# Kernel optimization log

Measured on AMD Instinct MI355X. Metric: run time of the kernel, lower is better.

Reference implementation:

```python
import jax, jax.numpy as jnp
import numpy as np

K = 3
PAD = 1
STRIDE = 1
DIL = 1


def _conv_offset(x, w, b):
    # standard 3x3 conv, NCHW
    out = jax.lax.conv_general_dilated(
        x, w, window_strides=(STRIDE, STRIDE), padding=((PAD, PAD), (PAD, PAD)),
        rhs_dilation=(DIL, DIL), dimension_numbers=('NCHW', 'OIHW', 'NCHW'))
    return out + b[None, :, None, None]


def _bilinear_sample(x, px, py):
    # x: (b,c,h,w); px,py: (b,N) absolute pixel coords; zero padding outside.
    b, c, h, w = x.shape
    x_flat = x.reshape(b, c, h * w)
    x0 = jnp.floor(px)
    y0 = jnp.floor(py)
    wx1 = px - x0
    wy1 = py - y0
    wx0 = 1.0 - wx1
    wy0 = 1.0 - wy1

    def gather(xi, yi, wt):
        valid = (xi >= 0) & (xi <= w - 1) & (yi >= 0) & (yi <= h - 1)
        xc = jnp.clip(xi, 0, w - 1).astype(jnp.int32)
        yc = jnp.clip(yi, 0, h - 1).astype(jnp.int32)
        idx = yc * w + xc  # (b,N)
        v = jax.vmap(lambda xf, i: jnp.take(xf, i, axis=1))(x_flat, idx)  # (b,c,N)
        return v * (wt * valid.astype(x.dtype))[:, None, :]

    out = gather(x0, y0, wy0 * wx0)
    out = out + gather(x0 + 1, y0, wy0 * wx1)
    out = out + gather(x0, y0 + 1, wy1 * wx0)
    out = out + gather(x0 + 1, y0 + 1, wy1 * wx1)
    return out


def setup_inputs() -> dict:
    key = jax.random.key(0)
    k1, k2, k3, k4 = jax.random.split(key, 4)
    x = jax.random.normal(k1, (8, 64, 128, 128), dtype=jnp.float32)
    # small random offset-predictor weights (repo inits to zero; random gives nonzero offsets)
    w_off = jax.random.normal(k2, (27, 64, 3, 3), dtype=jnp.float32) * 0.01
    b_off = jax.random.normal(k3, (27,), dtype=jnp.float32) * 0.01
    w_conv = jax.random.normal(k4, (64, 576), dtype=jnp.float32) / np.sqrt(3.0 * 576.0)
    return {"x": x, "w_off": w_off, "b_off": b_off, "w_conv": w_conv}


def reference(x, w_off, b_off, w_conv):
    b, c, h, w = x.shape
    out = _conv_offset(x, w_off, b_off)  # (b, 3*K*K, H, W)
    H, W = out.shape[2], out.shape[3]
    o1, o2, m = jnp.split(out, 3, axis=1)  # each (b, K*K, H, W)
    mask = jax.nn.sigmoid(m).reshape(b, 1, K, K, H, W)
    # base grid (absolute coords), per module __init__
    x_start = DIL / 2 * (K - 1) - PAD  # = 0.0 here
    y_start = DIL / 2 * (K - 1) - PAD
    x_cood = (x_start + STRIDE * jnp.arange(W)).astype(x.dtype)
    y_cood = (y_start + STRIDE * jnp.arange(H)).astype(x.dtype)
    # per-tap kernel bias, tap order is (kh, kw) row-major
    taps = (jnp.arange(K) - (K - 1) / 2) * DIL
    x_bias = jnp.tile(taps, K).astype(x.dtype)      # (K*K,)
    y_bias = jnp.repeat(taps, K).astype(x.dtype)    # (K*K,)
    px = o1 + x_cood[None, None, None, :] + x_bias[None, :, None, None]  # (b,9,H,W)
    py = o2 + y_cood[None, None, :, None] + y_bias[None, :, None, None]
    N = K * K * H * W
    y = _bilinear_sample(x, px.reshape(b, N), py.reshape(b, N))  # (b,c,N)
    y = y.reshape(b, c, K, K, H, W) * mask
    y = y.reshape(b, c * K * K, H, W)
    # 1x1 conv == channel GEMM
    return jnp.einsum('bkhw,ok->bohw', y, w_conv)
```

## Files before the change

kernel.cpp:

```cpp
#include <hip/hip_runtime.h>
#include <math.h>

#define HW_   128
#define CIN_  64
#define IMG_  (HW_ * HW_)

#define TR_    6
#define TC_    40
#define PIT_   36
#define TILEDW (TR_ * TC_ * PIT_)
#define NU_    (TR_ * 8 * 10)

typedef short    s16x8 __attribute__((ext_vector_type(8)));
typedef float    f32x4 __attribute__((ext_vector_type(4)));
typedef float    f32x2 __attribute__((ext_vector_type(2)));
typedef unsigned u32x4 __attribute__((ext_vector_type(4)));

__device__ __forceinline__ short f2bf(float f) {
  union { float f; unsigned i; } v; v.f = f;
  unsigned r = (v.i + 0x7fffu + ((v.i >> 16) & 1u)) >> 16;
  return (short)r;
}

#if defined(__has_builtin)
#if __has_builtin(__builtin_amdgcn_cvt_pk_bf16_f32)
#define HAVE_CVT_PK_BF16 1
#endif
#endif

__device__ __forceinline__ unsigned PK2(float a, float b) {
#ifdef HAVE_CVT_PK_BF16
  typedef __bf16 bf16x2_t __attribute__((ext_vector_type(2)));
  union { bf16x2_t v; unsigned u; } cv;
  cv.v = __builtin_amdgcn_cvt_pk_bf16_f32(a, b);
  return cv.u;
#else
  union { float f; unsigned u; } ua, ub; ua.f = a; ub.f = b;
  unsigned ra = ua.u + 0x7fffu + ((ua.u >> 16) & 1u);
  unsigned rb = ub.u + 0x7fffu + ((ub.u >> 16) & 1u);
  return __builtin_amdgcn_perm(rb, ra, 0x07060302u);
#endif
}

__device__ __forceinline__ f32x2 up2d(unsigned d) {
  union { unsigned u; float f; } lo, hi;
  lo.u = d << 16; hi.u = d;
  return (f32x2){lo.f, hi.f};
}


__global__ __launch_bounds__(256) void wprep(const float* __restrict__ w_off,
                                             const float* __restrict__ w_conv,
                                             short* __restrict__ wOf,
                                             short* __restrict__ wA) {
  int t = blockIdx.x * 256 + threadIdx.x;
  if (t < 36864) {
    int i = t & 7, o = (t >> 3) & 63, q = (t >> 9) & 3, ks = (t >> 11) & 1, j = t >> 12;
    int c = ks * 32 + q * 8 + i;
    wA[t] = f2bf(w_conv[o * 576 + c * 9 + j]);
  }
  if (t < 18432) {
    int i = t & 7, m = (t >> 3) & 31, q = (t >> 8) & 3, ks = (t >> 10) & 1, j = t >> 11;
    int c = ks * 32 + q * 8 + i;
    wOf[t] = (m < 27) ? f2bf(w_off[(m * 64 + c) * 9 + j]) : (short)0;
  }
}

__global__ __launch_bounds__(256)
__attribute__((amdgpu_waves_per_eu(4)))
void dfuse(const float* __restrict__ x,
           const short* __restrict__ wOf,
           const float* __restrict__ b_off,
           const short* __restrict__ wA,
           float* __restrict__ out) {
  __shared__ __align__(16) unsigned lds_[TILEDW];

  int bi  = blockIdx.x & 7;
  int tid = blockIdx.x >> 3;
  int h0  = (tid >> 2) << 1;
  int w0  = (tid & 3) << 5;
  int t   = threadIdx.x;
  int wv  = t >> 6, l = t & 63;
  int col = l & 15, q = l >> 4;
  int px_local = wv * 16 + col;
  int rl  = px_local >> 5;
  int cl  = px_local & 31;
  int h   = h0 + rl;
  int w   = w0 + cl;
  int p   = h * HW_ + w;

  const float* xB = x + (size_t)bi * (CIN_ * IMG_);

  {
    f32x4 L0a[4], L1a[4], L0b[4], L1b[4];
    int sda, sdb;
    unsigned ma, mb;
    {
      int u = t;
      int cc = u % 10, cq = (u / 10) & 7, r = u / 80;
      int y  = h0 - 2 + r;
      int ys = min(max(y, 0), HW_ - 1);
      int xg0 = w0 - 4 + cc * 4;
      int xs  = min(max(xg0, 0), HW_ - 4);
      ma = ((y >= 0) && (y < HW_) && (xg0 >= 0) && (xg0 < HW_)) ? 0xffffffffu : 0u;
      const float* s0 = xB + (size_t)(8 * cq) * IMG_ + ys * HW_ + xs;
#pragma unroll
      for (int i = 0; i < 4; ++i) {
        L0a[i] = *(const f32x4*)(s0 + (2 * i) * IMG_);
        L1a[i] = *(const f32x4*)(s0 + (2 * i + 1) * IMG_);
      }
      sda = (r * TC_ + cc * 4) * PIT_ + cq * 4;
    }
    bool hasB = (t + 256) < NU_;
    {
      int u = hasB ? (t + 256) : 0;
      int cc = u % 10, cq = (u / 10) & 7, r = u / 80;
      int y  = h0 - 2 + r;
      int ys = min(max(y, 0), HW_ - 1);
      int xg0 = w0 - 4 + cc * 4;
      int xs  = min(max(xg0, 0), HW_ - 4);
      mb = ((y >= 0) && (y < HW_) && (xg0 >= 0) && (xg0 < HW_)) ? 0xffffffffu : 0u;
      const float* s0 = xB + (size_t)(8 * cq) * IMG_ + ys * HW_ + xs;
#pragma unroll
      for (int i = 0; i < 4; ++i) {
        L0b[i] = *(const f32x4*)(s0 + (2 * i) * IMG_);
        L1b[i] = *(const f32x4*)(s0 + (2 * i + 1) * IMG_);
      }
      sdb = (r * TC_ + cc * 4) * PIT_ + cq * 4;
    }
#pragma unroll
    for (int pxi = 0; pxi < 4; ++pxi) {
      u32x4 v;
#pragma unroll
      for (int i = 0; i < 4; ++i) v[i] = PK2(L0a[i][pxi], L1a[i][pxi]) & ma;
      *(u32x4*)(lds_ + sda + pxi * PIT_) = v;
    }
    if (hasB) {
#pragma unroll
      for (int pxi = 0; pxi < 4; ++pxi) {
        u32x4 v;
#pragma unroll
        for (int i = 0; i < 4; ++i) v[i] = PK2(L0b[i][pxi], L1b[i][pxi]) & mb;
        *(u32x4*)(lds_ + sdb + pxi * PIT_) = v;
      }
    }
  }
  __syncthreads();

  float oall[32];
  {
    const short* wq = wOf + q * 256 + col * 8;
    f32x4 a0v = {0.f, 0.f, 0.f, 0.f};
    f32x4 a1v = {0.f, 0.f, 0.f, 0.f};
    f32x4 a0w = {0.f, 0.f, 0.f, 0.f};
    f32x4 a1w = {0.f, 0.f, 0.f, 0.f};
    const unsigned* tb = &lds_[((rl + 2) * TC_ + (cl + 4)) * PIT_ + q * 4];
#pragma unroll
    for (int j = 0; j < 9; ++j) {
      int dy = j / 3 - 1, dx = j % 3 - 1;
      const unsigned* tp = tb + (dy * TC_ + dx) * PIT_;
      union { u32x4 u; s16x8 v; } B0, B1;
      B0.u = *(const u32x4*)tp;
      B1.u = *(const u32x4*)(tp + 16);
      const short* wj = wq + j * 2048;
      s16x8 a00 = *(const s16x8*)(wj);
      s16x8 a01 = *(const s16x8*)(wj + 128);
      s16x8 a10 = *(const s16x8*)(wj + 1024);
      s16x8 a11 = *(const s16x8*)(wj + 1024 + 128);
      a0v = __builtin_amdgcn_mfma_f32_16x16x32_bf16(a00, B0.v, a0v, 0, 0, 0);
      a1v = __builtin_amdgcn_mfma_f32_16x16x32_bf16(a01, B0.v, a1v, 0, 0, 0);
      a0w = __builtin_amdgcn_mfma_f32_16x16x32_bf16(a10, B1.v, a0w, 0, 0, 0);
      a1w = __builtin_amdgcn_mfma_f32_16x16x32_bf16(a11, B1.v, a1w, 0, 0, 0);
    }
    a0v += a0w;
    a1v += a1w;
    float myv[8];
#pragma unroll
    for (int r = 0; r < 4; ++r) myv[r] = a0v[r] + b_off[q * 4 + r];
#pragma unroll
    for (int r = 0; r < 4; ++r) {
      int ch = 16 + q * 4 + r;
      float bo = b_off[min(ch, 26)];
      float v = a1v[r] + bo;
      myv[4 + r] = (ch >= 18) ? (1.f / (1.f + __expf(-v))) : v;
    }
#pragma unroll
    for (int qq = 0; qq < 4; ++qq) {
      int src = qq * 16 + col;
#pragma unroll
      for (int r = 0; r < 4; ++r) {
        oall[qq * 4 + r]      = __shfl(myv[r], src);
        oall[16 + qq * 4 + r] = __shfl(myv[4 + r], src);
      }
    }
  }

  f32x4 acc[4], accB[4];
#pragma unroll
  for (int ms = 0; ms < 4; ++ms) {
    acc[ms]  = (f32x4){0.f, 0.f, 0.f, 0.f};
    accB[ms] = (f32x4){0.f, 0.f, 0.f, 0.f};
  }

  const short* wqA = wA + q * 512 + col * 8;

#pragma unroll
  for (int j = 0; j < 9; ++j) {
    float o1 = oall[j], o2 = oall[9 + j], mk = oall[18 + j];

    float pxf = o1 + (float)(w + (j % 3) - 1);
    float pyf = o2 + (float)(h + (j / 3) - 1);
    float fx = floorf(pxf), fy = floorf(pyf);
    int   x0 = (int)fx,   y0 = (int)fy;
    float ax = pxf - fx, ay = pyf - fy;
    float bx = 1.f - ax, by = 1.f - ay;

    bx = (x0 >= 0  && x0 < HW_)     ? bx : 0.f;
    ax = (x0 >= -1 && x0 < HW_ - 1) ? ax : 0.f;
    by = (y0 >= 0  && y0 < HW_)     ? by : 0.f;
    ay = (y0 >= -1 && y0 < HW_ - 1) ? ay : 0.f;
    float bym = by * mk, aym = ay * mk;
    float u00 = bym * bx, u01 = bym * ax;
    float u10 = aym * bx, u11 = aym * ax;
    f32x2 U00 = {u00, u00}, U01 = {u01, u01};
    f32x2 U10 = {u10, u10}, U11 = {u11, u11};

    unsigned F0u[4], F1u[4];
    bool intile = (o1 >= -1.f) && (o1 < 1.f) && (o2 >= -1.f) && (o2 < 1.f);
    if (intile) {
      int r0 = y0 - (h0 - 2), c0 = x0 - (w0 - 4);
      const unsigned* t00 = &lds_[(r0 * TC_ + c0) * PIT_ + q * 4];
      u32x4 A00 = *(const u32x4*)(t00);
      u32x4 A01 = *(const u32x4*)(t00 + PIT_);
      u32x4 A10 = *(const u32x4*)(t00 + TC_ * PIT_);
      u32x4 A11 = *(const u32x4*)(t00 + TC_ * PIT_ + PIT_);
      u32x4 B00 = *(const u32x4*)(t00 + 16);
      u32x4 B01 = *(const u32x4*)(t00 + PIT_ + 16);
      u32x4 B10 = *(const u32x4*)(t00 + TC_ * PIT_ + 16);
      u32x4 B11 = *(const u32x4*)(t00 + TC_ * PIT_ + PIT_ + 16);
#pragma unroll
      for (int i = 0; i < 4; ++i) {
        f32x2 v0 = up2d(A00[i]) * U00 + up2d(A01[i]) * U01
                 + up2d(A10[i]) * U10 + up2d(A11[i]) * U11;
        F0u[i] = PK2(v0.x, v0.y);
        f32x2 v1 = up2d(B00[i]) * U00 + up2d(B01[i]) * U01
                 + up2d(B10[i]) * U10 + up2d(B11[i]) * U11;
        F1u[i] = PK2(v1.x, v1.y);
      }
    } else {
      int xc0 = min(max(x0, 0), HW_ - 1), xc1 = min(max(x0 + 1, 0), HW_ - 1);
      int yc0 = min(max(y0, 0), HW_ - 1), yc1 = min(max(y0 + 1, 0), HW_ - 1);
      int g00 = yc0 * HW_ + xc0, g01 = yc0 * HW_ + xc1;
      int g10 = yc1 * HW_ + xc0, g11 = yc1 * HW_ + xc1;
      for (int hB = 0; hB < 2; ++hB) {
        for (int ii = 0; ii < 4; ++ii) {
          int c0i = hB * 32 + q * 8 + 2 * ii;
          const float* pc = xB + c0i * IMG_;
          const float* pd = pc + IMG_;
          float va = u00 * pc[g00] + u01 * pc[g01] + u10 * pc[g10] + u11 * pc[g11];
          float vb = u00 * pd[g00] + u01 * pd[g01] + u10 * pd[g10] + u11 * pd[g11];
          if (hB) F1u[ii] = PK2(va, vb); else F0u[ii] = PK2(va, vb);
        }
      }
    }

    union { unsigned u[4]; s16x8 v; } F0, F1;
#pragma unroll
    for (int i = 0; i < 4; ++i) { F0.u[i] = F0u[i]; F1.u[i] = F1u[i]; }

    const short* wj = wqA + j * 4096;
#pragma unroll
    for (int ms = 0; ms < 4; ++ms) {
      s16x8 a0 = *(const s16x8*)(wj + ms * 128);
      acc[ms] = __builtin_amdgcn_mfma_f32_16x16x32_bf16(a0, F0.v, acc[ms], 0, 0, 0);
    }
#pragma unroll
    for (int ms = 0; ms < 4; ++ms) {
      s16x8 a1 = *(const s16x8*)(wj + 2048 + ms * 128);
      accB[ms] = __builtin_amdgcn_mfma_f32_16x16x32_bf16(a1, F1.v, accB[ms], 0, 0, 0);
    }
  }

  float* op = out + (size_t)bi * (CIN_ * IMG_) + p;
#pragma unroll
  for (int ms = 0; ms < 4; ++ms) {
    f32x4 r = acc[ms] + accB[ms];
#pragma unroll
    for (int rr = 0; rr < 4; ++rr)
      op[(ms * 16 + q * 4 + rr) * IMG_] = r[rr];
  }
}

extern "C" void kernel_launch(void* const* d_in, const int* in_sizes, int n_in,
                              void* d_out, int out_size, void* d_ws, size_t ws_size,
                              hipStream_t stream) {
  const float* x      = (const float*)d_in[0];
  const float* w_off  = (const float*)d_in[1];
  const float* b_off  = (const float*)d_in[2];
  const float* w_conv = (const float*)d_in[3];
  float* out = (float*)d_out;

  char* ws = (char*)d_ws;
  short* wOf = (short*)(ws);
  short* wA  = (short*)(ws + 36864);

  hipLaunchKernelGGL(wprep, dim3(144),  dim3(256), 0, stream, w_off, w_conv, wOf, wA);
  hipLaunchKernelGGL(dfuse, dim3(2048), dim3(256), 0, stream, x, wOf, b_off, wA, out);
}
```

Baseline: 125.8 us.

## XOR-swizzle LDS tile layout, drop padding, raise waves per EU

After: 164.0 us. 30.3% more time.

```diff
diff --git a/kernel.cpp b/kernel.cpp
--- a/kernel.cpp
+++ b/kernel.cpp
@@ -7,7 +7,7 @@
 
 #define TR_    6
 #define TC_    40
-#define PIT_   36
+#define PIT_   32
 #define TILEDW (TR_ * TC_ * PIT_)
 #define NU_    (TR_ * 8 * 10)
 
@@ -67,7 +67,7 @@
 }
 
 __global__ __launch_bounds__(256)
-__attribute__((amdgpu_waves_per_eu(4)))
+__attribute__((amdgpu_waves_per_eu(5)))
 void dfuse(const float* __restrict__ x,
            const short* __restrict__ wOf,
            const float* __restrict__ b_off,
@@ -93,7 +93,7 @@
 
   {
     f32x4 L0a[4], L1a[4], L0b[4], L1b[4];
-    int sda, sdb;
+    int baseA, baseB, swA, swB;
     unsigned ma, mb;
     {
       int u = t;
@@ -109,7 +109,8 @@
         L0a[i] = *(const f32x4*)(s0 + (2 * i) * IMG_);
         L1a[i] = *(const f32x4*)(s0 + (2 * i + 1) * IMG_);
       }
-      sda = (r * TC_ + cc * 4) * PIT_ + cq * 4;
+      baseA = (r * TC_ + cc * 4) * PIT_;
+      swA   = cq ^ ((cc & 1) << 2);
     }
     bool hasB = (t + 256) < NU_;
     {
@@ -126,14 +127,15 @@
         L0b[i] = *(const f32x4*)(s0 + (2 * i) * IMG_);
         L1b[i] = *(const f32x4*)(s0 + (2 * i + 1) * IMG_);
       }
-      sdb = (r * TC_ + cc * 4) * PIT_ + cq * 4;
+      baseB = (r * TC_ + cc * 4) * PIT_;
+      swB   = cq ^ ((cc & 1) << 2);
     }
 #pragma unroll
     for (int pxi = 0; pxi < 4; ++pxi) {
       u32x4 v;
 #pragma unroll
       for (int i = 0; i < 4; ++i) v[i] = PK2(L0a[i][pxi], L1a[i][pxi]) & ma;
-      *(u32x4*)(lds_ + sda + pxi * PIT_) = v;
+      *(u32x4*)(lds_ + baseA + pxi * PIT_ + ((swA ^ pxi) << 2)) = v;
     }
     if (hasB) {
 #pragma unroll
@@ -141,7 +143,7 @@
         u32x4 v;
 #pragma unroll
         for (int i = 0; i < 4; ++i) v[i] = PK2(L0b[i][pxi], L1b[i][pxi]) & mb;
-        *(u32x4*)(lds_ + sdb + pxi * PIT_) = v;
+        *(u32x4*)(lds_ + baseB + pxi * PIT_ + ((swB ^ pxi) << 2)) = v;
       }
     }
   }
@@ -149,20 +151,21 @@
 
   float oall[32];
   {
-    const short* wq = wOf + q * 256 + col * 8;
+    const short* wq_ = wOf + q * 256 + col * 8;
     f32x4 a0v = {0.f, 0.f, 0.f, 0.f};
     f32x4 a1v = {0.f, 0.f, 0.f, 0.f};
     f32x4 a0w = {0.f, 0.f, 0.f, 0.f};
     f32x4 a1w = {0.f, 0.f, 0.f, 0.f};
-    const unsigned* tb = &lds_[((rl + 2) * TC_ + (cl + 4)) * PIT_ + q * 4];
+    const unsigned* tbp = lds_ + ((rl + 2) * TC_ + (cl + 4)) * PIT_;
 #pragma unroll
     for (int j = 0; j < 9; ++j) {
       int dy = j / 3 - 1, dx = j % 3 - 1;
-      const unsigned* tp = tb + (dy * TC_ + dx) * PIT_;
+      int ca = (q ^ ((cl + 4 + dx) & 7)) << 2;
+      const unsigned* pb = tbp + (dy * TC_ + dx) * PIT_;
       union { u32x4 u; s16x8 v; } B0, B1;
-      B0.u = *(const u32x4*)tp;
-      B1.u = *(const u32x4*)(tp + 16);
-      const short* wj = wq + j * 2048;
+      B0.u = *(const u32x4*)(pb + ca);
+      B1.u = *(const u32x4*)(pb + (ca ^ 16));
+      const short* wj = wq_ + j * 2048;
       s16x8 a00 = *(const s16x8*)(wj);
       s16x8 a01 = *(const s16x8*)(wj + 128);
       s16x8 a10 = *(const s16x8*)(wj + 1024);
@@ -225,43 +228,52 @@
     f32x2 U00 = {u00, u00}, U01 = {u01, u01};
     f32x2 U10 = {u10, u10}, U11 = {u11, u11};
 
-    unsigned F0u[4], F1u[4];
+    u32x4 A00, A01, A10, A11, B00, B01, B10, B11;
     bool intile = (o1 >= -1.f) && (o1 < 1.f) && (o2 >= -1.f) && (o2 < 1.f);
     if (intile) {
       int r0 = y0 - (h0 - 2), c0 = x0 - (w0 - 4);
-      const unsigned* t00 = &lds_[(r0 * TC_ + c0) * PIT_ + q * 4];
-      u32x4 A00 = *(const u32x4*)(t00);
-      u32x4 A01 = *(const u32x4*)(t00 + PIT_);
-      u32x4 A10 = *(const u32x4*)(t00 + TC_ * PIT_);
-      u32x4 A11 = *(const u32x4*)(t00 + TC_ * PIT_ + PIT_);
-      u32x4 B00 = *(const u32x4*)(t00 + 16);
-      u32x4 B01 = *(const u32x4*)(t00 + PIT_ + 16);
-      u32x4 B10 = *(const u32x4*)(t00 + TC_ * PIT_ + 16);
-      u32x4 B11 = *(const u32x4*)(t00 + TC_ * PIT_ + PIT_ + 16);
-#pragma unroll
-      for (int i = 0; i < 4; ++i) {
-        f32x2 v0 = up2d(A00[i]) * U00 + up2d(A01[i]) * U01
-                 + up2d(A10[i]) * U10 + up2d(A11[i]) * U11;
-        F0u[i] = PK2(v0.x, v0.y);
-        f32x2 v1 = up2d(B00[i]) * U00 + up2d(B01[i]) * U01
-                 + up2d(B10[i]) * U10 + up2d(B11[i]) * U11;
-        F1u[i] = PK2(v1.x, v1.y);
-      }
+      const unsigned* b00 = lds_ + (r0 * TC_ + c0) * PIT_;
+      int s0 = (q ^ (c0 & 7)) << 2;
+      int s1 = (q ^ ((c0 + 1) & 7)) << 2;
+      A00 = *(const u32x4*)(b00 + s0);
+      A01 = *(const u32x4*)(b00 + PIT_ + s1);
+      A10 = *(const u32x4*)(b00 + TC_ * PIT_ + s0);
+      A11 = *(const u32x4*)(b00 + TC_ * PIT_ + PIT_ + s1);
+      B00 = *(const u32x4*)(b00 + (s0 ^ 16));
+      B01 = *(const u32x4*)(b00 + PIT_ + (s1 ^ 16));
+      B10 = *(const u32x4*)(b00 + TC_ * PIT_ + (s0 ^ 16));
+      B11 = *(const u32x4*)(b00 + TC_ * PIT_ + PIT_ + (s1 ^ 16));
     } else {
       int xc0 = min(max(x0, 0), HW_ - 1), xc1 = min(max(x0 + 1, 0), HW_ - 1);
       int yc0 = min(max(y0, 0), HW_ - 1), yc1 = min(max(y0 + 1, 0), HW_ - 1);
       int g00 = yc0 * HW_ + xc0, g01 = yc0 * HW_ + xc1;
       int g10 = yc1 * HW_ + xc0, g11 = yc1 * HW_ + xc1;
+#pragma unroll
       for (int hB = 0; hB < 2; ++hB) {
+#pragma unroll
         for (int ii = 0; ii < 4; ++ii) {
           int c0i = hB * 32 + q * 8 + 2 * ii;
           const float* pc = xB + c0i * IMG_;
           const float* pd = pc + IMG_;
-          float va = u00 * pc[g00] + u01 * pc[g01] + u10 * pc[g10] + u11 * pc[g11];
-          float vb = u00 * pd[g00] + u01 * pd[g01] + u10 * pd[g10] + u11 * pd[g11];
-          if (hB) F1u[ii] = PK2(va, vb); else F0u[ii] = PK2(va, vb);
+          unsigned v00 = PK2(pc[g00], pd[g00]);
+          unsigned v01 = PK2(pc[g01], pd[g01]);
+          unsigned v10 = PK2(pc[g10], pd[g10]);
+          unsigned v11 = PK2(pc[g11], pd[g11]);
+          if (hB) { B00[ii] = v00; B01[ii] = v01; B10[ii] = v10; B11[ii] = v11; }
+          else    { A00[ii] = v00; A01[ii] = v01; A10[ii] = v10; A11[ii] = v11; }
         }
       }
+    }
+
+    unsigned F0u[4], F1u[4];
+#pragma unroll
+    for (int i = 0; i < 4; ++i) {
+      f32x2 v0 = up2d(A00[i]) * U00 + up2d(A01[i]) * U01
+               + up2d(A10[i]) * U10 + up2d(A11[i]) * U11;
+      F0u[i] = PK2(v0.x, v0.y);
+      f32x2 v1 = up2d(B00[i]) * U00 + up2d(B01[i]) * U01
+               + up2d(B10[i]) * U10 + up2d(B11[i]) * U11;
+      F1u[i] = PK2(v1.x, v1.y);
     }
 
     union { unsigned u[4]; s16x8 v; } F0, F1;
```
